# Kernel optimization log

Hardware: AMD Instinct MI355X
Metric: run time of the kernel (lower is better)

The kernel has to match this reference:

```python
import jax, jax.numpy as jnp
import numpy as np

N = 4096
NEG = jnp.float32(-1e9)


def setup_inputs() -> dict:
    key = jax.random.key(0)
    ks = jax.random.split(key, 12)
    # sparse-ish adjacency (~20 neighbors/node) + self loops, as in GAT on PPI
    adj = (jax.random.uniform(ks[0], (N, N)) < 0.005).astype(jnp.int32)
    adj = adj.at[jnp.arange(N), jnp.arange(N)].set(1)
    x = jax.random.normal(ks[1], (N, 50), dtype=jnp.float32)
    def w(k, shape, fan_in):
        return jax.random.normal(k, shape, dtype=jnp.float32) * (1.0 / np.sqrt(fan_in))
    return {
        "x": x, "adj": adj,
        "W1": w(ks[2], (4, 50, 256), 50),   "a1s": w(ks[3], (4, 256), 256),  "a1d": w(ks[4], (4, 256), 256),
        "W2": w(ks[5], (4, 1024, 256), 1024), "a2s": w(ks[6], (4, 256), 256),  "a2d": w(ks[7], (4, 256), 256),
        "W3": w(ks[8], (6, 1024, 121), 1024), "a3s": w(ks[9], (6, 121), 121), "a3d": w(ks[10], (6, 121), 121),
    }


def gat_layer(x, mask, W, a_src, a_dst, concat):
    # x: [N, F_in], W: [H, F_in, F_out]
    h = jnp.einsum('nf,hfo->hno', x, W)                    # [H, N, F_out]
    es = jnp.einsum('hno,ho->hn', h, a_src)                # per-source score
    ed = jnp.einsum('hno,ho->hn', h, a_dst)                # per-dest score
    e = jax.nn.leaky_relu(es[:, :, None] + ed[:, None, :], 0.2)  # [H, N, N]
    e = jnp.where(mask[None], e, NEG)
    alpha = jax.nn.softmax(e, axis=-1)                     # masked neighbor softmax
    out = jnp.einsum('hnm,hmo->hno', alpha, h)             # aggregate neighbors
    if concat:
        return out.transpose(1, 0, 2).reshape(out.shape[1], -1)  # [N, H*F_out]
    return out.mean(axis=0)                                # [N, F_out]


def reference(x, adj, W1, a1s, a1d, W2, a2s, a2d, W3, a3s, a3d):
    mask = adj > 0
    x1 = jax.nn.elu(gat_layer(x, mask, W1, a1s, a1d, concat=True))           # [N, 1024]
    x2 = jax.nn.elu(gat_layer(x1, mask, W2, a2s, a2d, concat=True)) + x1     # residual
    x3 = jax.nn.log_softmax(gat_layer(x2, mask, W3, a3s, a3d, concat=False), axis=1)
    return x3
```

## Files before the change

### kernel.cpp

```cpp
#include <hip/hip_runtime.h>
#include <hip/hip_bf16.h>
#include <math.h>

#define NNODES 4096
#define MAXD 128
#define PSTR (6 * NNODES)

typedef __attribute__((ext_vector_type(8))) short bf16x8;
typedef __attribute__((ext_vector_type(4))) float f32x4;
typedef __attribute__((ext_vector_type(2))) float f32x2;
typedef __attribute__((ext_vector_type(16))) float f32x16;
typedef __attribute__((ext_vector_type(4))) ushort u16x4;

__device__ inline ushort f32_to_bf16_rne(float f) {
    uint32_t u = __float_as_uint(f);
    u += 0x7FFFu + ((u >> 16) & 1u);
    return (ushort)(u >> 16);
}
__device__ inline float bf16_to_f32(ushort h) {
    return __uint_as_float((uint32_t)h << 16);
}
__device__ inline f32x4 u4_to_f32(u16x4 v) {
    f32x4 r;
    r[0] = bf16_to_f32(v[0]); r[1] = bf16_to_f32(v[1]);
    r[2] = bf16_to_f32(v[2]); r[3] = bf16_to_f32(v[3]);
    return r;
}

__global__ __launch_bounds__(256) void pre_kern(const int* __restrict__ adj,
                                                int* __restrict__ deg,
                                                int* __restrict__ nbr,
                                                const float* __restrict__ x,
                                                const float* __restrict__ W1,
                                                const float* __restrict__ W2,
                                                const float* __restrict__ W3,
                                                ushort* __restrict__ Xhi,
                                                ushort* __restrict__ W1h,
                                                ushort* __restrict__ W2h,
                                                ushort* __restrict__ W3h) {
    __shared__ float tile[32][33];
    __shared__ int cnts[256];
    int id = blockIdx.x;
    int tid = threadIdx.x;
    if (id < 4096) {
        int n = id;
        const int* row = adj + (size_t)n * NNODES;
        int c0 = tid * 16;
        int vals[16];
        const int4* r4 = (const int4*)(row + c0);
#pragma unroll
        for (int i = 0; i < 4; i++) {
            int4 v = r4[i];
            vals[4 * i] = v.x; vals[4 * i + 1] = v.y; vals[4 * i + 2] = v.z; vals[4 * i + 3] = v.w;
        }
        int cnt = 0;
#pragma unroll
        for (int i = 0; i < 16; i++) cnt += (vals[i] != 0) ? 1 : 0;
        cnts[tid] = cnt;
        __syncthreads();
        if (tid == 0) {
            int s = 0;
            for (int i = 0; i < 256; i++) { int c = cnts[i]; cnts[i] = s; s += c; }
            deg[n] = (s < MAXD) ? s : MAXD;
        }
        __syncthreads();
        int o = cnts[tid];
        int* outr = nbr + (size_t)n * MAXD;
#pragma unroll
        for (int i = 0; i < 16; i++) {
            if (vals[i] != 0) {
                if (o < MAXD) outr[o] = c0 + i;
                o++;
            }
        }
        return;
    }
    id -= 4096;
    if (id >= 1856) {
        int i = (id - 1856) * 256 + tid;
        int k = i & 63;
        int m = i >> 6;
        float v = (k < 50) ? x[(size_t)m * 50 + k] : 0.f;
        Xhi[i] = f32_to_bf16_rne(v);
        return;
    }
    const float* W; ushort* Whi;
    int h, r, K, KP, N, NP, gy;
    if (id < 64)        { W = W1; Whi = W1h; K = 50;   KP = 64;   N = 256; NP = 256; h = id / 16;           r = id % 16;         gy = 8; }
    else if (id < 1088) { W = W2; Whi = W2h; K = 1024; KP = 1024; N = 256; NP = 256; h = (id - 64) / 256;   r = (id - 64) % 256; gy = 8; }
    else                { W = W3; Whi = W3h; K = 1024; KP = 1024; N = 121; NP = 128; h = (id - 1088) / 128; r = (id - 1088) % 128; gy = 4; }
    int k0 = (r / gy) * 32, n0 = (r % gy) * 32;
    const float* Wh_ = W + (size_t)h * K * N;
#pragma unroll
    for (int q = 0; q < 4; q++) {
        int kl = (tid >> 5) + q * 8;
        int nl = tid & 31;
        int k = k0 + kl, n = n0 + nl;
        tile[kl][nl] = (k < K && n < N) ? Wh_[(size_t)k * N + n] : 0.f;
    }
    __syncthreads();
#pragma unroll
    for (int q = 0; q < 4; q++) {
        int nl = (tid >> 5) + q * 8;
        int kl = tid & 31;
        size_t o = ((size_t)h * NP + n0 + nl) * KP + k0 + kl;
        Whi[o] = f32_to_bf16_rne(tile[kl][nl]);
    }
}

__global__ __launch_bounds__(256, 1) void gemm_mfma(const ushort* __restrict__ Xhi,
                                                    const ushort* __restrict__ Whi,
                                                    ushort* __restrict__ Hb,
                                                    const float* __restrict__ AsrcAll,
                                                    const float* __restrict__ AdstAll,
                                                    float* __restrict__ esp,
                                                    float* __restrict__ edp,
                                                    int KP, int NP, int Nstride, int Nreal,
                                                    int nby) {
    extern __shared__ ushort lds[];
    constexpr int AH = 0, BH = 9216, BUF = 18432;
    int b = blockIdx.x;
    int perx = gridDim.x >> 3;
    int g = (b & 7) * perx + (b >> 3);
    int per_head = 32 * nby;
    int h = g / per_head;
    int r0 = g - h * per_head;
    const int m0 = (r0 / nby) * 128;
    const int n0 = (r0 % nby) * 128;
    const int blkj = n0 >> 7;
    const int tid = threadIdx.x;
    const int lane = tid & 63;
    const int w = tid >> 6;
    const int wr = (w >> 1) * 64, wc = (w & 1) * 64;
    const int fr = lane & 31;
    const int fg = lane >> 5;
    const ushort* Wh_ = Whi + (size_t)h * NP * KP;
    const int sr = tid >> 3;
    const int sc8 = (tid & 7) * 8;
    bf16x8 pa[4], pb[4];
    auto LOADG = [&](int K0) {
#pragma unroll
        for (int i = 0; i < 4; i++) {
            pa[i] = *(const bf16x8*)&Xhi[(size_t)(m0 + sr + 32 * i) * KP + K0 + sc8];
            pb[i] = *(const bf16x8*)&Wh_[(size_t)(n0 + sr + 32 * i) * KP + K0 + sc8];
        }
    };
    LOADG(0);
    f32x16 acc[2][2] = {};
    int cur = 0;
    for (int k0 = 0; k0 < KP; k0 += 64) {
        const int bo = cur * BUF;
#pragma unroll
        for (int i = 0; i < 4; i++) {
            int r = (sr + 32 * i) * 72 + sc8;
            *(bf16x8*)&lds[bo + AH + r] = pa[i];
            *(bf16x8*)&lds[bo + BH + r] = pb[i];
        }
        if (k0 + 64 < KP) LOADG(k0 + 64);
        __syncthreads();
#pragma unroll
        for (int ks = 0; ks < 4; ks++) {
            const int kc = ks * 16 + fg * 8;
            bf16x8 ah[2], bh[2];
#pragma unroll
            for (int i = 0; i < 2; i++) {
                ah[i] = *(const bf16x8*)&lds[bo + AH + (wr + i * 32 + fr) * 72 + kc];
                bh[i] = *(const bf16x8*)&lds[bo + BH + (wc + i * 32 + fr) * 72 + kc];
            }
#pragma unroll
            for (int i = 0; i < 2; i++)
#pragma unroll
                for (int j = 0; j < 2; j++)
                    acc[i][j] = __builtin_amdgcn_mfma_f32_32x32x16_bf16(ah[i], bh[j], acc[i][j], 0, 0, 0);
        }
        cur ^= 1;
    }
#pragma unroll
    for (int i = 0; i < 2; i++)
#pragma unroll
        for (int j = 0; j < 2; j++)
#pragma unroll
            for (int reg = 0; reg < 16; reg++) {
                int row = m0 + wr + i * 32 + (reg & 3) + 8 * (reg >> 2) + 4 * fg;
                int col = n0 + wc + j * 32 + fr;
                Hb[((size_t)h * NNODES + row) * Nstride + col] = f32_to_bf16_rne(acc[i][j][reg]);
            }
    __syncthreads();
    float* fl = (float*)lds;
    constexpr int EDO = 2 * 128 * 34;
    const float* Asrc = AsrcAll + (size_t)h * Nreal;
    const float* Adst = AdstAll + (size_t)h * Nreal;
    float as_[2], ad_[2];
#pragma unroll
    for (int j = 0; j < 2; j++) {
        int col = n0 + wc + j * 32 + fr;
        as_[j] = (col < Nreal) ? Asrc[col] : 0.f;
        ad_[j] = (col < Nreal) ? Adst[col] : 0.f;
    }
    const int wcidx = (w & 1);
#pragma unroll
    for (int i = 0; i < 2; i++)
#pragma unroll
        for (int reg = 0; reg < 16; reg++) {
            int row = wr + i * 32 + (reg & 3) + 8 * (reg >> 2) + 4 * fg;
            float pe = acc[i][0][reg] * as_[0] + acc[i][1][reg] * as_[1];
            float pd = acc[i][0][reg] * ad_[0] + acc[i][1][reg] * ad_[1];
            fl[(wcidx * 128 + row) * 34 + fr] = pe;
            fl[EDO + (wcidx * 128 + row) * 34 + fr] = pd;
        }
    __syncthreads();
    if (tid < 128) {
        int r = tid;
        float s = 0.f;
#pragma unroll
        for (int q = 0; q < 32; q++)
            s += fl[r * 34 + q] + fl[(128 + r) * 34 + q];
        esp[(size_t)blkj * PSTR + h * NNODES + m0 + r] = s;
    } else {
        int r = tid - 128;
        float s = 0.f;
#pragma unroll
        for (int q = 0; q < 32; q++)
            s += fl[EDO + r * 34 + q] + fl[EDO + (128 + r) * 34 + q];
        edp[(size_t)blkj * PSTR + h * NNODES + m0 + r] = s;
    }
}

template<int HEADS, int NPARTS, bool RES>
__global__ __launch_bounds__(256) void aggregate_kern(const ushort* __restrict__ Hb,
                                                      const float* __restrict__ esp,
                                                      const float* __restrict__ edp,
                                                      const int* __restrict__ deg,
                                                      const int* __restrict__ nbr,
                                                      ushort* outHi) {
    constexpr int FOUT = 256;
    int b = blockIdx.x;
    int g = (b & 7) * ((HEADS * NNODES / 4) / 8) + (b >> 3);
    int h = g / (NNODES / 4);
    int n = (g % (NNODES / 4)) * 4 + (threadIdx.x >> 6);
    int lane = threadIdx.x & 63;
    int d = deg[n];
    const int* nb = nbr + (size_t)n * MAXD;
    float esn = esp[h * NNODES + n];
    if (NPARTS == 2) esn += esp[PSTR + h * NNODES + n];
    float sc[2];
    int nm[2];
    float mx = -INFINITY;
#pragma unroll
    for (int r = 0; r < 2; r++) {
        int j = lane + r * 64;
        int m = (j < d) ? nb[j] : 0;
        nm[r] = m;
        float e = -INFINITY;
        if (j < d) {
            float t = esn + edp[h * NNODES + m];
            if (NPARTS == 2) t += edp[PSTR + h * NNODES + m];
            e = (t > 0.f) ? t : 0.2f * t;
        }
        sc[r] = e;
        mx = fmaxf(mx, e);
    }
#pragma unroll
    for (int sh = 32; sh >= 1; sh >>= 1) mx = fmaxf(mx, __shfl_xor(mx, sh));
    float sum = 0.f;
#pragma unroll
    for (int r = 0; r < 2; r++) {
        float ex = (sc[r] == -INFINITY) ? 0.f : expf(sc[r] - mx);
        sc[r] = ex;
        sum += ex;
    }
#pragma unroll
    for (int sh = 32; sh >= 1; sh >>= 1) sum += __shfl_xor(sum, sh);
    float inv = 1.f / sum;
    sc[0] *= inv; sc[1] *= inv;
    const ushort* Hh = Hb + (size_t)h * NNODES * FOUT;
    f32x4 ac0 = {}, ac1 = {}, ac2 = {}, ac3 = {};
    int j = 0;
    for (; j + 3 < d; j += 4) {
        float a0 = __shfl(sc[j >> 6], j & 63);
        int q0 = __shfl(nm[j >> 6], j & 63);
        float a1 = __shfl(sc[(j + 1) >> 6], (j + 1) & 63);
        int q1 = __shfl(nm[(j + 1) >> 6], (j + 1) & 63);
        float a2 = __shfl(sc[(j + 2) >> 6], (j + 2) & 63);
        int q2 = __shfl(nm[(j + 2) >> 6], (j + 2) & 63);
        float a3 = __shfl(sc[(j + 3) >> 6], (j + 3) & 63);
        int q3 = __shfl(nm[(j + 3) >> 6], (j + 3) & 63);
        u16x4 v0 = *(const u16x4*)&Hh[(size_t)q0 * FOUT + lane * 4];
        u16x4 v1 = *(const u16x4*)&Hh[(size_t)q1 * FOUT + lane * 4];
        u16x4 v2 = *(const u16x4*)&Hh[(size_t)q2 * FOUT + lane * 4];
        u16x4 v3 = *(const u16x4*)&Hh[(size_t)q3 * FOUT + lane * 4];
        ac0 += a0 * u4_to_f32(v0);
        ac1 += a1 * u4_to_f32(v1);
        ac2 += a2 * u4_to_f32(v2);
        ac3 += a3 * u4_to_f32(v3);
    }
    for (; j < d; j++) {
        float a0 = __shfl(sc[j >> 6], j & 63);
        int q0 = __shfl(nm[j >> 6], j & 63);
        u16x4 v0 = *(const u16x4*)&Hh[(size_t)q0 * FOUT + lane * 4];
        ac0 += a0 * u4_to_f32(v0);
    }
    f32x4 acc = (ac0 + ac1) + (ac2 + ac3);
    size_t idx = (size_t)n * (HEADS * FOUT) + (size_t)h * FOUT + lane * 4;
    u16x4 hi4, rh;
    if (RES) rh = *(const u16x4*)&outHi[idx];
#pragma unroll
    for (int i = 0; i < 4; i++) {
        float v = acc[i];
        v = (v > 0.f) ? v : (expf(v) - 1.f);
        if (RES) v += bf16_to_f32(rh[i]);
        hi4[i] = f32_to_bf16_rne(v);
    }
    *(u16x4*)&outHi[idx] = hi4;
}

__global__ __launch_bounds__(256) void aggregate3a_kern(const ushort* __restrict__ Hb,
                                                        const float* __restrict__ esp,
                                                        const float* __restrict__ edp,
                                                        const int* __restrict__ deg,
                                                        const int* __restrict__ nbr,
                                                        float* __restrict__ agg) {
    constexpr int HEADS = 6;
    int b = blockIdx.x;
    int g = (b & 7) * ((HEADS * NNODES / 4) / 8) + (b >> 3);
    int h = g / (NNODES / 4);
    int n = (g % (NNODES / 4)) * 4 + (threadIdx.x >> 6);
    int lane = threadIdx.x & 63;
    int d = deg[n];
    const int* nb = nbr + (size_t)n * MAXD;
    float esn = esp[h * NNODES + n];
    float sc[2];
    int nm[2];
    float mx = -INFINITY;
#pragma unroll
    for (int r = 0; r < 2; r++) {
        int j = lane + r * 64;
        int m = (j < d) ? nb[j] : 0;
        nm[r] = m;
        float e = -INFINITY;
        if (j < d) {
            float t = esn + edp[h * NNODES + m];
            e = (t > 0.f) ? t : 0.2f * t;
        }
        sc[r] = e;
        mx = fmaxf(mx, e);
    }
#pragma unroll
    for (int sh = 32; sh >= 1; sh >>= 1) mx = fmaxf(mx, __shfl_xor(mx, sh));
    float sum = 0.f;
#pragma unroll
    for (int r = 0; r < 2; r++) {
        float ex = (sc[r] == -INFINITY) ? 0.f : expf(sc[r] - mx);
        sc[r] = ex;
        sum += ex;
    }
#pragma unroll
    for (int sh = 32; sh >= 1; sh >>= 1) sum += __shfl_xor(sum, sh);
    float inv = 1.f / sum;
    sc[0] *= inv; sc[1] *= inv;
    const ushort* Hh = Hb + (size_t)h * NNODES * 128;
    int c0 = lane * 2;
    f32x2 ac0 = {}, ac1 = {}, ac2 = {}, ac3 = {};
    auto LD = [&](int q) -> f32x2 {
        uint vv = *(const uint*)&Hh[(size_t)q * 128 + c0];
        f32x2 r;
        r[0] = bf16_to_f32((ushort)(vv & 0xffffu));
        r[1] = bf16_to_f32((ushort)(vv >> 16));
        return r;
    };
    int j = 0;
    for (; j + 3 < d; j += 4) {
        float a0 = __shfl(sc[j >> 6], j & 63);
        int q0 = __shfl(nm[j >> 6], j & 63);
        float a1 = __shfl(sc[(j + 1) >> 6], (j + 1) & 63);
        int q1 = __shfl(nm[(j + 1) >> 6], (j + 1) & 63);
        float a2 = __shfl(sc[(j + 2) >> 6], (j + 2) & 63);
        int q2 = __shfl(nm[(j + 2) >> 6], (j + 2) & 63);
        float a3 = __shfl(sc[(j + 3) >> 6], (j + 3) & 63);
        int q3 = __shfl(nm[(j + 3) >> 6], (j + 3) & 63);
        ac0 += a0 * LD(q0);
        ac1 += a1 * LD(q1);
        ac2 += a2 * LD(q2);
        ac3 += a3 * LD(q3);
    }
    for (; j < d; j++) {
        float a0 = __shfl(sc[j >> 6], j & 63);
        int q0 = __shfl(nm[j >> 6], j & 63);
        ac0 += a0 * LD(q0);
    }
    f32x2 acc = (ac0 + ac1) + (ac2 + ac3);
    *(f32x2*)&agg[((size_t)h * NNODES + n) * 128 + c0] = acc;
}

__global__ __launch_bounds__(256) void reduce3_kern(const float* __restrict__ agg,
                                                    float* __restrict__ outp) {
    constexpr int FOUT = 121;
    int n = blockIdx.x * 4 + (threadIdx.x >> 6);
    int lane = threadIdx.x & 63;
    int c0 = lane * 2;
    f32x2 l = {};
#pragma unroll
    for (int h = 0; h < 6; h++)
        l += *(const f32x2*)&agg[((size_t)h * NNODES + n) * 128 + c0];
    l = l * (1.f / 6.f);
    float m0 = (c0 < FOUT) ? l[0] : -INFINITY;
    float m1 = (c0 + 1 < FOUT) ? l[1] : -INFINITY;
    float mx = fmaxf(m0, m1);
#pragma unroll
    for (int sh = 32; sh >= 1; sh >>= 1) mx = fmaxf(mx, __shfl_xor(mx, sh));
    float s = ((c0 < FOUT) ? expf(l[0] - mx) : 0.f) + ((c0 + 1 < FOUT) ? expf(l[1] - mx) : 0.f);
#pragma unroll
    for (int sh = 32; sh >= 1; sh >>= 1) s += __shfl_xor(s, sh);
    float lse = logf(s);
    if (c0 < FOUT) outp[(size_t)n * FOUT + c0] = l[0] - mx - lse;
    if (c0 + 1 < FOUT) outp[(size_t)n * FOUT + c0 + 1] = l[1] - mx - lse;
}

extern "C" void kernel_launch(void* const* d_in, const int* in_sizes, int n_in,
                              void* d_out, int out_size, void* d_ws, size_t ws_size,
                              hipStream_t stream) {
    const float* x   = (const float*)d_in[0];
    const int*   adj = (const int*)d_in[1];
    const float* W1  = (const float*)d_in[2];
    const float* a1s = (const float*)d_in[3];
    const float* a1d = (const float*)d_in[4];
    const float* W2  = (const float*)d_in[5];
    const float* a2s = (const float*)d_in[6];
    const float* a2d = (const float*)d_in[7];
    const float* W3  = (const float*)d_in[8];
    const float* a3s = (const float*)d_in[9];
    const float* a3d = (const float*)d_in[10];
    float* outp = (float*)d_out;

    char* w = (char*)d_ws;
    int* deg = (int*)w;      w += (size_t)NNODES * sizeof(int);
    int* nbr = (int*)w;      w += (size_t)NNODES * MAXD * sizeof(int);
    ushort* hbuf = (ushort*)w; w += (size_t)4 * NNODES * 256 * sizeof(ushort);
    float* esp = (float*)w;  w += (size_t)2 * PSTR * sizeof(float);
    float* edp = (float*)w;  w += (size_t)2 * PSTR * sizeof(float);
    ushort* Xhi = (ushort*)w; w += (size_t)NNODES * 1024 * sizeof(ushort);
    ushort* W1h = (ushort*)w; w += (size_t)4 * 256 * 64 * sizeof(ushort);
    ushort* W2h = (ushort*)w; w += (size_t)4 * 256 * 1024 * sizeof(ushort);
    ushort* W3h = (ushort*)w; w += (size_t)6 * 128 * 1024 * sizeof(ushort);
    float* agg = (float*)w;  w += (size_t)6 * NNODES * 128 * sizeof(float);

    constexpr size_t GEMM_LDS = 2u * 2u * 128u * 72u * sizeof(ushort);

    pre_kern<<<6976, 256, 0, stream>>>(adj, deg, nbr, x, W1, W2, W3,
                                       Xhi, W1h, W2h, W3h);

    gemm_mfma<<<256, 256, GEMM_LDS, stream>>>(Xhi, W1h, hbuf,
                                              a1s, a1d, esp, edp, 64, 256, 256, 256, 2);
    aggregate_kern<4, 2, false><<<4 * NNODES / 4, 256, 0, stream>>>(
        hbuf, esp, edp, deg, nbr, Xhi);

    gemm_mfma<<<256, 256, GEMM_LDS, stream>>>(Xhi, W2h, hbuf,
                                              a2s, a2d, esp, edp, 1024, 256, 256, 256, 2);
    aggregate_kern<4, 2, true><<<4 * NNODES / 4, 256, 0, stream>>>(
        hbuf, esp, edp, deg, nbr, Xhi);

    gemm_mfma<<<192, 256, GEMM_LDS, stream>>>(Xhi, W3h, hbuf,
                                              a3s, a3d, esp, edp, 1024, 128, 128, 121, 1);
    aggregate3a_kern<<<6 * NNODES / 4, 256, 0, stream>>>(hbuf, esp, edp, deg, nbr, agg);
    reduce3_kern<<<NNODES / 4, 256, 0, stream>>>(agg, outp);
}
```

Measured before the change: 119.9 us.

## Stage GEMM tiles with direct global-to-LDS loads and XOR swizzle

Replaces the register-staged global loads followed by LDS stores in the MFMA GEMM with direct global_load_lds transfers into a double-buffered LDS tile. The padded 72-element row stride gives way to an unpadded 64-element layout with an XOR swizzle on 16-byte chunks to avoid bank conflicts. The barrier moves to the end of each k-iteration so the next tile's prefetch overlaps the current MFMA work. This removes VGPR pressure and LDS write instructions, but relies on the async loads completing before the trailing barrier, which the code does not wait on explicitly.

```diff
diff --git a/kernel.cpp b/kernel.cpp
--- a/kernel.cpp
+++ b/kernel.cpp
@@ -118,7 +118,7 @@
                                                     int KP, int NP, int Nstride, int Nreal,
                                                     int nby) {
     extern __shared__ ushort lds[];
-    constexpr int AH = 0, BH = 9216, BUF = 18432;
+    constexpr int AH = 0, BH = 8192, BUF = 16384;
     int b = blockIdx.x;
     int perx = gridDim.x >> 3;
     int g = (b & 7) * perx + (b >> 3);
@@ -135,37 +135,41 @@
     const int fr = lane & 31;
     const int fg = lane >> 5;
     const ushort* Wh_ = Whi + (size_t)h * NP * KP;
-    const int sr = tid >> 3;
-    const int sc8 = (tid & 7) * 8;
-    bf16x8 pa[4], pb[4];
-    auto LOADG = [&](int K0) {
+    auto STAGE = [&](int buf, int K0) {
 #pragma unroll
         for (int i = 0; i < 4; i++) {
-            pa[i] = *(const bf16x8*)&Xhi[(size_t)(m0 + sr + 32 * i) * KP + K0 + sc8];
-            pb[i] = *(const bf16x8*)&Wh_[(size_t)(n0 + sr + 32 * i) * KP + K0 + sc8];
+            int c = w * 64 + i * 256 + lane;
+            int row = c >> 3;
+            int lc = (c & 7) ^ (row & 7);
+            const ushort* ga = &Xhi[(size_t)(m0 + row) * KP + K0 + lc * 8];
+            const ushort* gb = &Wh_[(size_t)(n0 + row) * KP + K0 + lc * 8];
+            ushort* la = &lds[buf * BUF + AH + (w * 64 + i * 256) * 8];
+            ushort* lb = &lds[buf * BUF + BH + (w * 64 + i * 256) * 8];
+            __builtin_amdgcn_global_load_lds(
+                (const __attribute__((address_space(1))) uint32_t*)ga,
+                (__attribute__((address_space(3))) uint32_t*)la, 16, 0, 0);
+            __builtin_amdgcn_global_load_lds(
+                (const __attribute__((address_space(1))) uint32_t*)gb,
+                (__attribute__((address_space(3))) uint32_t*)lb, 16, 0, 0);
         }
     };
-    LOADG(0);
+    STAGE(0, 0);
+    __syncthreads();
     f32x16 acc[2][2] = {};
     int cur = 0;
     for (int k0 = 0; k0 < KP; k0 += 64) {
+        if (k0 + 64 < KP) STAGE(cur ^ 1, k0 + 64);
         const int bo = cur * BUF;
 #pragma unroll
-        for (int i = 0; i < 4; i++) {
-            int r = (sr + 32 * i) * 72 + sc8;
-            *(bf16x8*)&lds[bo + AH + r] = pa[i];
-            *(bf16x8*)&lds[bo + BH + r] = pb[i];
-        }
-        if (k0 + 64 < KP) LOADG(k0 + 64);
-        __syncthreads();
-#pragma unroll
         for (int ks = 0; ks < 4; ks++) {
-            const int kc = ks * 16 + fg * 8;
+            const int pc = (ks * 2 + fg) ^ (fr & 7);
             bf16x8 ah[2], bh[2];
 #pragma unroll
             for (int i = 0; i < 2; i++) {
-                ah[i] = *(const bf16x8*)&lds[bo + AH + (wr + i * 32 + fr) * 72 + kc];
-                bh[i] = *(const bf16x8*)&lds[bo + BH + (wc + i * 32 + fr) * 72 + kc];
+                int rowA = wr + i * 32 + fr;
+                ah[i] = *(const bf16x8*)&lds[bo + AH + rowA * 64 + pc * 8];
+                int rowB = wc + i * 32 + fr;
+                bh[i] = *(const bf16x8*)&lds[bo + BH + rowB * 64 + pc * 8];
             }
 #pragma unroll
             for (int i = 0; i < 2; i++)
@@ -173,6 +177,7 @@
                 for (int j = 0; j < 2; j++)
                     acc[i][j] = __builtin_amdgcn_mfma_f32_32x32x16_bf16(ah[i], bh[j], acc[i][j], 0, 0, 0);
         }
+        __syncthreads();
         cur ^= 1;
     }
 #pragma unroll
@@ -444,7 +449,7 @@
     ushort* W3h = (ushort*)w; w += (size_t)6 * 128 * 1024 * sizeof(ushort);
     float* agg = (float*)w;  w += (size_t)6 * NNODES * 128 * sizeof(float);
 
-    constexpr size_t GEMM_LDS = 2u * 2u * 128u * 72u * sizeof(ushort);
+    constexpr size_t GEMM_LDS = 73728;
 
     pre_kern<<<6976, 256, 0, stream>>>(adj, deg, nbr, x, W1, W2, W3,
                                        Xhi, W1h, W2h, W3h);
```

Result: no change. 121.7 us (+1.6%).
